# Performance work log

Hardware: AMD Instinct MI355X
Metric: run time of the kernel (lower is better)

## Reference

```python
import jax, jax.numpy as jnp
import numpy as np

NUM_CLS = 80
C = 256
IMG = 1024.0
N = 256
SR = 2  # sampling_ratio
MIN_SIZE = 16.0
SCALES = (0.25, 0.125, 0.0625, 0.03125)
HW = ((256, 256), (128, 128), (64, 64), (32, 32))


def _roialign(feat, rois, scale, out):
    # feat: [C, H, W]; rois: [n, 4] (y1, x1, y2, x2) in image coords.
    # torchvision-style ROIAlign (aligned=False), sampling_ratio=SR, avg pool.
    Cc, H, W = feat.shape
    n = rois.shape[0]
    y1 = rois[:, 0] * scale
    x1 = rois[:, 1] * scale
    rh = jnp.maximum(rois[:, 2] * scale - y1, 1.0)
    rw = jnp.maximum(rois[:, 3] * scale - x1, 1.0)
    # per-bin sample offsets: (bin + (s+0.5)/SR) * bin_size
    g = (jnp.arange(out, dtype=feat.dtype)[:, None]
         + (jnp.arange(SR, dtype=feat.dtype)[None, :] + 0.5) / SR).reshape(-1)  # [out*SR]
    ys = y1[:, None] + g[None, :] * (rh / out)[:, None]  # [n, out*SR]
    xs = x1[:, None] + g[None, :] * (rw / out)[:, None]
    S = out * SR
    yy = jnp.broadcast_to(ys[:, :, None], (n, S, S)).reshape(n, S * S)
    xx = jnp.broadcast_to(xs[:, None, :], (n, S, S)).reshape(n, S * S)
    valid = (yy > -1.0) & (yy < H) & (xx > -1.0) & (xx < W)
    yc = jnp.clip(yy, 0.0, H - 1.0)
    xc = jnp.clip(xx, 0.0, W - 1.0)
    y0 = jnp.floor(yc)
    x0 = jnp.floor(xc)
    ly = yc - y0
    lx = xc - x0
    y0i = y0.astype(jnp.int32)
    x0i = x0.astype(jnp.int32)
    y1i = jnp.minimum(y0i + 1, H - 1)
    x1i = jnp.minimum(x0i + 1, W - 1)
    f00 = feat[:, y0i, x0i]  # [C, n, S*S]
    f01 = feat[:, y0i, x1i]
    f10 = feat[:, y1i, x0i]
    f11 = feat[:, y1i, x1i]
    val = (f00 * (1 - ly) * (1 - lx) + f01 * (1 - ly) * lx
           + f10 * ly * (1 - lx) + f11 * ly * lx)
    val = jnp.where(valid[None], val, 0.0)
    val = val.reshape(Cc, n, out, SR, out, SR).mean(axis=(3, 5))
    return val.transpose(1, 0, 2, 3)  # [n, C, out, out]


def _pool(P, rois, out):
    # roi_layer: FPN level assignment via log2 of sqrt(area)/224, clamp to levels 0..3
    area = jnp.prod(rois[:, 2:4] - rois[:, 0:2] + 1.0, axis=-1)
    lvl = jnp.clip(jnp.floor(4.0 + jnp.log(jnp.sqrt(area) / 224.0) / np.log(2.0)), 2.0, 5.0) - 2.0
    lvl = lvl.astype(jnp.int32)
    pooled = jnp.zeros((rois.shape[0], C, out, out), dtype=rois.dtype)
    for l in range(4):
        pl = _roialign(P[l], rois, SCALES[l], out)
        pooled = pooled + jnp.where((lvl == l)[:, None, None, None], pl, 0.0)
    return pooled


def _loc2bbox(loc, anchor):
    chw = anchor[..., 2:4] - anchor[..., 0:2]
    cyx = anchor[..., 0:2] + chw * 0.5
    yx = loc[..., 0:2] * chw + cyx
    hw = jnp.exp(loc[..., 2:4]) * chw
    return jnp.concatenate([yx - hw * 0.5, yx + hw * 0.5], axis=-1)


def _head(x, W1, b1, W2, b2, Wc, bc, Wl, bl):
    x = x.reshape(x.shape[0], -1)
    h = jax.nn.relu(x @ W1 + b1)
    h = jax.nn.relu(h @ W2 + b2)
    return h @ Wc + bc, h @ Wl + bl


def _cascade(P, rois, params):
    stds = (jnp.array([0.1, 0.1, 0.2, 0.2], dtype=rois.dtype),
            jnp.array([0.05, 0.05, 0.1, 0.1], dtype=rois.dtype),
            jnp.array([1 / 30.0, 1 / 30.0, 1 / 15.0, 1 / 15.0], dtype=rois.dtype))
    roi = rois
    valid = jnp.ones((rois.shape[0],), dtype=bool)
    t = jnp.arange(rois.shape[0])
    pre_b = jnp.zeros((rois.shape[0], NUM_CLS, 4), dtype=rois.dtype)
    pre_s = jnp.zeros((rois.shape[0], NUM_CLS), dtype=rois.dtype)
    for s in range(3):
        x = _pool(P, roi, 7)
        logits, loc = _head(x, *params[s])
        loc = loc.reshape(-1, NUM_CLS + 1, 4)[:, 1:] * stds[s]
        boxes = _loc2bbox(loc, roi[:, None, :])  # [N, NUM_CLS, 4]
        score = jax.nn.softmax(logits, axis=-1)[:, 1:]
        pre_b = pre_b + boxes
        pre_s = pre_s + score
        best = jnp.argmax(score, axis=-1)
        roi = boxes[t, best]
        roi = jnp.clip(roi, 0.0, IMG)  # square image: clamp both coords to [0, IMG]
        if s < 2:  # original filters only after stages 1 and 2
            hw = roi[:, 2:4] - roi[:, 0:2]
            valid = valid & jnp.all(hw >= MIN_SIZE, axis=-1)
    m = valid.astype(pre_s.dtype)
    return pre_b / 3.0 * m[:, None, None], pre_s / 3.0 * m[:, None]


def setup_inputs():
    key = jax.random.key(0)
    ks = jax.random.split(key, 32)
    inp = {}
    for i, (h, w) in enumerate(HW):
        inp[f"P{i}"] = jax.random.normal(ks[i], (C, h, w), dtype=jnp.float32)
    yx1 = jax.random.uniform(ks[4], (N, 2), minval=0.0, maxval=IMG - 64.0)
    sz = jnp.exp(jax.random.uniform(ks[5], (N, 2), minval=np.log(16.0), maxval=np.log(600.0)))
    yx2 = jnp.clip(yx1 + sz, 0.0, IMG - 1.0)
    inp["rois"] = jnp.concatenate([yx1, yx2], axis=-1).astype(jnp.float32)
    dims = [(C * 49, 1024), (1024,), (1024, 1024), (1024,),
            (1024, NUM_CLS + 1), (NUM_CLS + 1,), (1024, (NUM_CLS + 1) * 4), ((NUM_CLS + 1) * 4,)]
    names = ["W1", "b1", "W2", "b2", "Wc", "bc", "Wl", "bl"]
    k = 6
    for s in range(3):
        for nm, d in zip(names, dims):
            if len(d) == 1:
                inp[f"s{s}_{nm}"] = jnp.zeros(d, dtype=jnp.float32)
            else:
                inp[f"s{s}_{nm}"] = 0.02 * jax.random.normal(ks[k], d, dtype=jnp.float32)
                k += 1
    return inp


def reference(P0, P1, P2, P3, rois,
              s0_W1, s0_b1, s0_W2, s0_b2, s0_Wc, s0_bc, s0_Wl, s0_bl,
              s1_W1, s1_b1, s1_W2, s1_b2, s1_Wc, s1_bc, s1_Wl, s1_bl,
              s2_W1, s2_b1, s2_W2, s2_b2, s2_Wc, s2_bc, s2_Wl, s2_bl):
    P = (P0, P1, P2, P3)
    params = [(s0_W1, s0_b1, s0_W2, s0_b2, s0_Wc, s0_bc, s0_Wl, s0_bl),
              (s1_W1, s1_b1, s1_W2, s1_b2, s1_Wc, s1_bc, s1_Wl, s1_bl),
              (s2_W1, s2_b1, s2_W2, s2_b2, s2_Wc, s2_bc, s2_Wl, s2_bl)]
    return _cascade(P, rois, params)
```

## Files before the change

kernel.cpp:

```cpp
#include <hip/hip_runtime.h>
#include <math.h>


#define NROI 256
#define NCLS 80
#define APITCH 40

typedef __attribute__((ext_vector_type(8))) short short8;
typedef __attribute__((ext_vector_type(4))) float f32x4;

__device__ __forceinline__ unsigned short f2bf(float f) {
  unsigned u = __builtin_bit_cast(unsigned, f);
  unsigned r = (u + 0x7FFFu + ((u >> 16) & 1u)) >> 16;
  return (unsigned short)r;
}
__device__ __forceinline__ float bf2f(unsigned short u) {
  return __builtin_bit_cast(float, (unsigned)u << 16);
}

__global__ __launch_bounds__(256) void prep_kernel(
    const float* __restrict__ P0, const float* __restrict__ P1,
    const float* __restrict__ P2, const float* __restrict__ P3,
    unsigned short* __restrict__ Pb0, unsigned short* __restrict__ Pb1,
    unsigned short* __restrict__ Pb2, unsigned short* __restrict__ Pb3,
    const float* __restrict__ W1a, const float* __restrict__ W1b,
    const float* __restrict__ W1c,
    const float* __restrict__ W2a, const float* __restrict__ W2b,
    const float* __restrict__ W2c,
    const float* __restrict__ Wca, const float* __restrict__ Wcb,
    const float* __restrict__ Wcc,
    const float* __restrict__ Wla, const float* __restrict__ Wlb,
    const float* __restrict__ Wlc,
    unsigned short* __restrict__ Wt1, unsigned short* __restrict__ Wt2,
    unsigned short* __restrict__ Wth) {
  __shared__ unsigned short tile[32][33];
  int bid = blockIdx.x;
  int t = threadIdx.x;
  int r = t >> 3;
  int c4 = (t & 7) * 4;

  float4 v;
  unsigned short* dptr;

  if (bid < 21760) {
    const float* S;
    unsigned short* D;
    int N, idx;
    if (bid < 16384)      { S = P0; D = Pb0; N = 65536; idx = bid; }
    else if (bid < 20480) { S = P1; D = Pb1; N = 16384; idx = bid - 16384; }
    else if (bid < 21504) { S = P2; D = Pb2; N = 4096;  idx = bid - 20480; }
    else                  { S = P3; D = Pb3; N = 1024;  idx = bid - 21504; }
    int k0 = (idx & 7) * 32;
    int n0 = (idx >> 3) * 32;
    v = *(const float4*)(S + (size_t)(k0 + r) * N + n0 + c4);
    dptr = D + (size_t)(n0 + r) * 256 + k0 + c4;
  } else if (bid < 59392) {
    int idx = bid - 21760;
    int s = idx / 12544;
    idx -= s * 12544;
    const float* W = (s == 0) ? W1a : (s == 1) ? W1b : W1c;
    int bx = idx % 392;
    int by = idx / 392;
    int kd0 = bx * 32;
    int n0 = by * 32;
    int p = kd0 >> 8;
    int c0 = kd0 & 255;
    v = *(const float4*)(W + (size_t)((c0 + r) * 49 + p) * 1024 + n0 + c4);
    dptr = Wt1 + (size_t)s * 12544 * 1024 + (size_t)(n0 + r) * 12544 + kd0 + c4;
  } else if (bid < 62464) {
    int idx = bid - 59392;
    int s = idx >> 10;
    idx &= 1023;
    const float* W = (s == 0) ? W2a : (s == 1) ? W2b : W2c;
    int k0 = (idx & 31) * 32;
    int n0 = (idx >> 5) * 32;
    v = *(const float4*)(W + (size_t)(k0 + r) * 1024 + n0 + c4);
    dptr = Wt2 + (size_t)s * 1024 * 1024 + (size_t)(n0 + r) * 1024 + k0 + c4;
  } else {
    int idx = bid - 62464;
    int s = idx >> 9;
    idx &= 511;
    const float* wc = (s == 0) ? Wca : (s == 1) ? Wcb : Wcc;
    const float* wl = (s == 0) ? Wla : (s == 1) ? Wlb : Wlc;
    int k0 = (idx & 31) * 32;
    int n0 = (idx >> 5) * 32;
    float vv[4];
#pragma unroll
    for (int j = 0; j < 4; j++) {
      int nn = n0 + c4 + j;
      float x = 0.0f;
      if (nn < 81) x = wc[(size_t)(k0 + r) * 81 + nn];
      else if (nn < 405) x = wl[(size_t)(k0 + r) * 324 + (nn - 81)];
      vv[j] = x;
    }
    v.x = vv[0]; v.y = vv[1]; v.z = vv[2]; v.w = vv[3];
    dptr = Wth + (size_t)s * 512 * 1024 + (size_t)(n0 + r) * 1024 + k0 + c4;
  }

  tile[r][c4 + 0] = f2bf(v.x);
  tile[r][c4 + 1] = f2bf(v.y);
  tile[r][c4 + 2] = f2bf(v.z);
  tile[r][c4 + 3] = f2bf(v.w);
  __syncthreads();
  struct __attribute__((aligned(8))) US4 { unsigned short a, b, c, d; } o;
  o.a = tile[c4 + 0][r];
  o.b = tile[c4 + 1][r];
  o.c = tile[c4 + 2][r];
  o.d = tile[c4 + 3][r];
  *(US4*)dptr = o;
}

__global__ __launch_bounds__(256) void pool_kernel2(
    const unsigned short* __restrict__ Pb0, const unsigned short* __restrict__ Pb1,
    const unsigned short* __restrict__ Pb2, const unsigned short* __restrict__ Pb3,
    const float* __restrict__ roi, unsigned short* __restrict__ pooled) {
  int t = threadIdx.x;
  int n = blockIdx.y;
  int p = blockIdx.x * 4 + (t >> 6);
  if (p >= 49) return;
  int lane = t & 63;
  int c4 = lane * 4;
  int py = p / 7, px = p % 7;

  float r0 = roi[n * 4 + 0];
  float r1 = roi[n * 4 + 1];
  float r2 = roi[n * 4 + 2];
  float r3 = roi[n * 4 + 3];

  float area = (r2 - r0 + 1.0f) * (r3 - r1 + 1.0f);
  float lf = floorf(4.0f + log2f(sqrtf(area) / 224.0f));
  lf = fminf(fmaxf(lf, 2.0f), 5.0f);
  int lvl = (int)lf - 2;

  float scale;
  int H;
  const unsigned short* fb;
  if (lvl == 0)      { scale = 0.25f;    H = 256; fb = Pb0; }
  else if (lvl == 1) { scale = 0.125f;   H = 128; fb = Pb1; }
  else if (lvl == 2) { scale = 0.0625f;  H = 64;  fb = Pb2; }
  else               { scale = 0.03125f; H = 32;  fb = Pb3; }
  int W = H;

  float y1 = r0 * scale;
  float x1 = r1 * scale;
  float rh = fmaxf(r2 * scale - y1, 1.0f);
  float rw = fmaxf(r3 * scale - x1, 1.0f);
  float bh = rh * (1.0f / 7.0f);
  float bw = rw * (1.0f / 7.0f);

  float a0 = 0.f, a1 = 0.f, a2 = 0.f, a3 = 0.f;
#pragma unroll
  for (int ry = 0; ry < 2; ry++) {
    float yy = y1 + ((float)py + ((float)ry + 0.5f) * 0.5f) * bh;
    bool vy = (yy > -1.0f) && (yy < (float)H);
    float ycl = fminf(fmaxf(yy, 0.0f), (float)(H - 1));
    float y0f = floorf(ycl);
    float ly = ycl - y0f;
    int y0i = (int)y0f;
    int y1i = min(y0i + 1, H - 1);
#pragma unroll
    for (int rx = 0; rx < 2; rx++) {
      float xx = x1 + ((float)px + ((float)rx + 0.5f) * 0.5f) * bw;
      bool vx = (xx > -1.0f) && (xx < (float)W);
      float xcl = fminf(fmaxf(xx, 0.0f), (float)(W - 1));
      float x0f = floorf(xcl);
      float lx = xcl - x0f;
      int x0i = (int)x0f;
      int x1i = min(x0i + 1, W - 1);
      float w00 = (1.f - ly) * (1.f - lx);
      float w01 = (1.f - ly) * lx;
      float w10 = ly * (1.f - lx);
      float w11 = ly * lx;
      if (!(vy && vx)) { w00 = w01 = w10 = w11 = 0.f; }
      ushort4 f00 = *(const ushort4*)(fb + ((size_t)(y0i * W + x0i) * 256 + c4));
      ushort4 f01 = *(const ushort4*)(fb + ((size_t)(y0i * W + x1i) * 256 + c4));
      ushort4 f10 = *(const ushort4*)(fb + ((size_t)(y1i * W + x0i) * 256 + c4));
      ushort4 f11 = *(const ushort4*)(fb + ((size_t)(y1i * W + x1i) * 256 + c4));
      a0 += bf2f(f00.x) * w00 + bf2f(f01.x) * w01 + bf2f(f10.x) * w10 + bf2f(f11.x) * w11;
      a1 += bf2f(f00.y) * w00 + bf2f(f01.y) * w01 + bf2f(f10.y) * w10 + bf2f(f11.y) * w11;
      a2 += bf2f(f00.z) * w00 + bf2f(f01.z) * w01 + bf2f(f10.z) * w10 + bf2f(f11.z) * w11;
      a3 += bf2f(f00.w) * w00 + bf2f(f01.w) * w01 + bf2f(f10.w) * w10 + bf2f(f11.w) * w11;
    }
  }
  ushort4 o;
  o.x = f2bf(a0 * 0.25f);
  o.y = f2bf(a1 * 0.25f);
  o.z = f2bf(a2 * 0.25f);
  o.w = f2bf(a3 * 0.25f);
  *(ushort4*)(pooled + (size_t)n * 12544 + p * 256 + c4) = o;
}

__global__ __launch_bounds__(256) void gemm_bf16(
    const unsigned short* __restrict__ A, const unsigned short* __restrict__ B,
    float* __restrict__ Cpart, int M, int N, int K, int iters) {
  __shared__ unsigned short As[128 * APITCH];
  __shared__ unsigned short Bs[128 * APITCH];
  const int t = threadIdx.x;
  const int n0 = blockIdx.x * 128;
  const int m0 = blockIdx.y * 128;
  const size_t kt0 = (size_t)blockIdx.z * iters * 32;

  const int row = t >> 2;
  const int off = (t & 3) * 8;
  const unsigned short* pa0 = A + (size_t)(m0 + row) * K + kt0 + off;
  const unsigned short* pa1 = pa0 + (size_t)64 * K;
  const unsigned short* pb0 = B + (size_t)(n0 + row) * K + kt0 + off;
  const unsigned short* pb1 = pb0 + (size_t)64 * K;

  const int lane = t & 63;
  const int wave = t >> 6;
  const int wm = (wave >> 1) * 64;
  const int wn = (wave & 1) * 64;
  const int fr = lane & 15;
  const int kq = (lane >> 4) * 8;

  f32x4 acc[4][4];
#pragma unroll
  for (int i = 0; i < 4; i++)
#pragma unroll
    for (int j = 0; j < 4; j++) acc[i][j] = (f32x4){0.f, 0.f, 0.f, 0.f};

  uint4 ra0 = *(const uint4*)pa0;
  uint4 ra1 = *(const uint4*)pa1;
  uint4 rb0 = *(const uint4*)pb0;
  uint4 rb1 = *(const uint4*)pb1;

  for (int it = 0; it < iters; ++it) {
    *(uint4*)&As[row * APITCH + off] = ra0;
    *(uint4*)&As[(row + 64) * APITCH + off] = ra1;
    *(uint4*)&Bs[row * APITCH + off] = rb0;
    *(uint4*)&Bs[(row + 64) * APITCH + off] = rb1;
    __syncthreads();
    if (it + 1 < iters) {
      int d = (it + 1) * 32;
      ra0 = *(const uint4*)(pa0 + d);
      ra1 = *(const uint4*)(pa1 + d);
      rb0 = *(const uint4*)(pb0 + d);
      rb1 = *(const uint4*)(pb1 + d);
    }
    short8 af[4], bfv[4];
#pragma unroll
    for (int f = 0; f < 4; f++)
      af[f] = *(const short8*)&As[(wm + f * 16 + fr) * APITCH + kq];
#pragma unroll
    for (int f = 0; f < 4; f++)
      bfv[f] = *(const short8*)&Bs[(wn + f * 16 + fr) * APITCH + kq];
#pragma unroll
    for (int fm = 0; fm < 4; fm++)
#pragma unroll
      for (int fn = 0; fn < 4; fn++)
        acc[fm][fn] = __builtin_amdgcn_mfma_f32_16x16x32_bf16(af[fm], bfv[fn],
                                                              acc[fm][fn], 0, 0, 0);
    __syncthreads();
  }

  float* Cp = Cpart + (size_t)blockIdx.z * M * N;
  const int colb = n0 + wn + fr;
  const int rowb = m0 + wm + (lane >> 4) * 4;
#pragma unroll
  for (int fm = 0; fm < 4; fm++)
#pragma unroll
    for (int fn = 0; fn < 4; fn++)
#pragma unroll
      for (int r = 0; r < 4; r++)
        Cp[(size_t)(rowb + fm * 16 + r) * N + (colb + fn * 16)] = acc[fm][fn][r];
}

__global__ __launch_bounds__(256) void reduce_bias_relu(
    const float* __restrict__ parts, int nparts, const float* __restrict__ bias,
    unsigned short* __restrict__ outb) {
  int i = blockIdx.x * 256 + threadIdx.x;
  float s = 0.0f;
  for (int p = 0; p < nparts; ++p) s += parts[(size_t)p * 262144 + i];
  s = fmaxf(s + bias[i & 1023], 0.0f);
  outb[i] = f2bf(s);
}

__global__ __launch_bounds__(128) void decode_kernel(
    const float* __restrict__ headp, const float* __restrict__ bc,
    const float* __restrict__ bl,
    const float* __restrict__ roi_in, float* __restrict__ roi_out,
    float* __restrict__ valid,
    float* __restrict__ pre_b, float* __restrict__ pre_s,
    float* __restrict__ out,
    float st0, float st1, float st2, float st3, int stage) {
  int n = blockIdx.x;
  int t = threadIdx.x;
  __shared__ float red[128];
  __shared__ int redi[128];
  __shared__ float sroi[4];
  __shared__ float boxes[NCLS][4];

  if (t < 4) sroi[t] = roi_in[n * 4 + t];
  float l = -INFINITY;
  if (t < 81) {
    float s = 0.f;
#pragma unroll
    for (int z = 0; z < 4; z++) s += headp[(size_t)z * 131072 + n * 512 + t];
    l = s + bc[t];
  }
  red[t] = l;
  __syncthreads();
#pragma unroll
  for (int s = 64; s > 0; s >>= 1) {
    if (t < s) red[t] = fmaxf(red[t], red[t + s]);
    __syncthreads();
  }
  float mx = red[0];
  __syncthreads();
  red[t] = (t < 81) ? expf(l - mx) : 0.0f;
  __syncthreads();
#pragma unroll
  for (int s = 64; s > 0; s >>= 1) {
    if (t < s) red[t] += red[t + s];
    __syncthreads();
  }
  float denom = red[0];
  __syncthreads();

  float score = -INFINITY;
  if (t < NCLS) {
    float lj = 0.f;
#pragma unroll
    for (int z = 0; z < 4; z++) lj += headp[(size_t)z * 131072 + n * 512 + (t + 1)];
    lj += bc[t + 1];
    score = expf(lj - mx) / denom;
    float lp[4];
#pragma unroll
    for (int j = 0; j < 4; j++) {
      float s = 0.f;
#pragma unroll
      for (int z = 0; z < 4; z++)
        s += headp[(size_t)z * 131072 + n * 512 + 81 + (t + 1) * 4 + j];
      lp[j] = s + bl[(t + 1) * 4 + j];
    }
    float dy = lp[0] * st0;
    float dx = lp[1] * st1;
    float dh = lp[2] * st2;
    float dw = lp[3] * st3;
    float h_ = sroi[2] - sroi[0];
    float w_ = sroi[3] - sroi[1];
    float cy = sroi[0] + h_ * 0.5f;
    float cx = sroi[1] + w_ * 0.5f;
    float ny = dy * h_ + cy;
    float nx = dx * w_ + cx;
    float nh = expf(dh) * h_;
    float nw = expf(dw) * w_;
    float b0 = ny - nh * 0.5f;
    float b1v = nx - nw * 0.5f;
    float b2v = ny + nh * 0.5f;
    float b3v = nx + nw * 0.5f;
    int o = (n * NCLS + t) * 4;
    if (stage == 0) {
      pre_b[o + 0] = b0;
      pre_b[o + 1] = b1v;
      pre_b[o + 2] = b2v;
      pre_b[o + 3] = b3v;
      pre_s[n * NCLS + t] = score;
    } else if (stage == 1) {
      pre_b[o + 0] += b0;
      pre_b[o + 1] += b1v;
      pre_b[o + 2] += b2v;
      pre_b[o + 3] += b3v;
      pre_s[n * NCLS + t] += score;
    } else {
      float vm = valid[n] * (1.0f / 3.0f);
      out[o + 0] = (pre_b[o + 0] + b0) * vm;
      out[o + 1] = (pre_b[o + 1] + b1v) * vm;
      out[o + 2] = (pre_b[o + 2] + b2v) * vm;
      out[o + 3] = (pre_b[o + 3] + b3v) * vm;
      out[NROI * NCLS * 4 + n * NCLS + t] = (pre_s[n * NCLS + t] + score) * vm;
    }
    if (stage < 2) {
      boxes[t][0] = b0;
      boxes[t][1] = b1v;
      boxes[t][2] = b2v;
      boxes[t][3] = b3v;
    }
  }
  if (stage < 2) {
    red[t] = score;
    redi[t] = t;
    __syncthreads();
    for (int s = 64; s > 0; s >>= 1) {
      if (t < s) {
        float o2 = red[t + s];
        int oi = redi[t + s];
        if (o2 > red[t] || (o2 == red[t] && oi < redi[t])) {
          red[t] = o2;
          redi[t] = oi;
        }
      }
      __syncthreads();
    }
    if (t == 0) {
      int best = redi[0];
      float ry1 = fminf(fmaxf(boxes[best][0], 0.0f), 1024.0f);
      float rx1 = fminf(fmaxf(boxes[best][1], 0.0f), 1024.0f);
      float ry2 = fminf(fmaxf(boxes[best][2], 0.0f), 1024.0f);
      float rx2 = fminf(fmaxf(boxes[best][3], 0.0f), 1024.0f);
      roi_out[n * 4 + 0] = ry1;
      roi_out[n * 4 + 1] = rx1;
      roi_out[n * 4 + 2] = ry2;
      roi_out[n * 4 + 3] = rx2;
      float hh = ry2 - ry1, ww = rx2 - rx1;
      bool ok = (hh >= 16.0f && ww >= 16.0f);
      if (stage == 0) valid[n] = ok ? 1.0f : 0.0f;
      else if (!ok) valid[n] = 0.0f;
    }
  }
}

extern "C" void kernel_launch(void* const* d_in, const int* in_sizes, int n_in,
                              void* d_out, int out_size, void* d_ws, size_t ws_size,
                              hipStream_t stream) {
  const float* P0 = (const float*)d_in[0];
  const float* P1 = (const float*)d_in[1];
  const float* P2 = (const float*)d_in[2];
  const float* P3 = (const float*)d_in[3];
  const float* rois = (const float*)d_in[4];
  float* out = (float*)d_out;
  float* ws = (float*)d_ws;

  float* roi   = ws;
  float* valid = roi + 1024;
  float* pre_b = valid + 256;
  float* pre_s = pre_b + 81920;
  float* part1 = pre_s + 20480;
  float* part2 = part1 + (size_t)14 * 262144;
  float* parth = part2 + (size_t)8 * 262144;
  unsigned short* pooledb = (unsigned short*)(parth + (size_t)4 * 131072);
  unsigned short* Wt1 = pooledb + (size_t)256 * 12544;
  unsigned short* Wt2 = Wt1 + (size_t)3 * 12544 * 1024;
  unsigned short* Wth = Wt2 + (size_t)3 * 1024 * 1024;
  unsigned short* h1b = Wth + (size_t)3 * 512 * 1024;
  unsigned short* h2b = h1b + (size_t)256 * 1024;
  unsigned short* Pb0 = h2b + (size_t)256 * 1024;
  unsigned short* Pb1 = Pb0 + (size_t)65536 * 256;
  unsigned short* Pb2 = Pb1 + (size_t)16384 * 256;
  unsigned short* Pb3 = Pb2 + (size_t)4096 * 256;

  prep_kernel<<<64000, 256, 0, stream>>>(
      P0, P1, P2, P3, Pb0, Pb1, Pb2, Pb3,
      (const float*)d_in[5 + 0 * 8 + 0], (const float*)d_in[5 + 1 * 8 + 0],
      (const float*)d_in[5 + 2 * 8 + 0],
      (const float*)d_in[5 + 0 * 8 + 2], (const float*)d_in[5 + 1 * 8 + 2],
      (const float*)d_in[5 + 2 * 8 + 2],
      (const float*)d_in[5 + 0 * 8 + 4], (const float*)d_in[5 + 1 * 8 + 4],
      (const float*)d_in[5 + 2 * 8 + 4],
      (const float*)d_in[5 + 0 * 8 + 6], (const float*)d_in[5 + 1 * 8 + 6],
      (const float*)d_in[5 + 2 * 8 + 6],
      Wt1, Wt2, Wth);

  const float stds[3][4] = {
      {0.1f, 0.1f, 0.2f, 0.2f},
      {0.05f, 0.05f, 0.1f, 0.1f},
      {1.0f / 30.0f, 1.0f / 30.0f, 1.0f / 15.0f, 1.0f / 15.0f}};

  for (int s = 0; s < 3; s++) {
    const float* b1 = (const float*)d_in[5 + s * 8 + 1];
    const float* b2 = (const float*)d_in[5 + s * 8 + 3];
    const float* bc = (const float*)d_in[5 + s * 8 + 5];
    const float* bl = (const float*)d_in[5 + s * 8 + 7];
    const float* roi_src = (s == 0) ? rois : roi;

    pool_kernel2<<<dim3(13, 256), 256, 0, stream>>>(Pb0, Pb1, Pb2, Pb3, roi_src,
                                                    pooledb);

    gemm_bf16<<<dim3(8, 2, 14), 256, 0, stream>>>(
        pooledb, Wt1 + (size_t)s * 12544 * 1024, part1, 256, 1024, 12544, 28);
    reduce_bias_relu<<<1024, 256, 0, stream>>>(part1, 14, b1, h1b);

    gemm_bf16<<<dim3(8, 2, 8), 256, 0, stream>>>(
        h1b, Wt2 + (size_t)s * 1024 * 1024, part2, 256, 1024, 1024, 4);
    reduce_bias_relu<<<1024, 256, 0, stream>>>(part2, 8, b2, h2b);

    gemm_bf16<<<dim3(4, 2, 4), 256, 0, stream>>>(
        h2b, Wth + (size_t)s * 512 * 1024, parth, 256, 512, 1024, 8);

    decode_kernel<<<256, 128, 0, stream>>>(parth, bc, bl, roi_src, roi, valid,
                                           pre_b, pre_s, out, stds[s][0],
                                           stds[s][1], stds[s][2], stds[s][3], s);
  }
}
```

Baseline: 481.3 us.

## Replace split-K GEMMs for FC2/head with fused bias-ReLU GEMM, widen prep tiles

Adds a 64x64-tile MFMA GEMM without split-K that applies bias and ReLU in its epilogue. It replaces the split-K FC2 GEMM plus reduce kernel and the split-K head GEMM, so decode now reads a single partial. This removes two launches per stage and the fp32 partial-buffer round trips, at the cost of fewer blocks in flight over the K=1024 loop. The prep transpose kernel also handles two 32x32 tiles per block with vectorized LDS writes, halving its block count.

Result: slower. 511.0 us (+6.2%).

```diff
diff --git a/kernel.cpp b/kernel.cpp
--- a/kernel.cpp
+++ b/kernel.cpp
@@ -17,6 +17,8 @@
 __device__ __forceinline__ float bf2f(unsigned short u) {
   return __builtin_bit_cast(float, (unsigned)u << 16);
 }
+
+struct __attribute__((aligned(8))) US4 { unsigned short a, b, c, d; };
 
 __global__ __launch_bounds__(256) void prep_kernel(
     const float* __restrict__ P0, const float* __restrict__ P1,
@@ -33,81 +35,103 @@
     const float* __restrict__ Wlc,
     unsigned short* __restrict__ Wt1, unsigned short* __restrict__ Wt2,
     unsigned short* __restrict__ Wth) {
-  __shared__ unsigned short tile[32][33];
+  __shared__ unsigned short tile[2][32][36];
   int bid = blockIdx.x;
   int t = threadIdx.x;
   int r = t >> 3;
   int c4 = (t & 7) * 4;
 
-  float4 v;
-  unsigned short* dptr;
-
-  if (bid < 21760) {
+  float4 v0, v1;
+  unsigned short *dp0, *dp1;
+
+  if (bid < 10880) {
     const float* S;
     unsigned short* D;
     int N, idx;
-    if (bid < 16384)      { S = P0; D = Pb0; N = 65536; idx = bid; }
-    else if (bid < 20480) { S = P1; D = Pb1; N = 16384; idx = bid - 16384; }
-    else if (bid < 21504) { S = P2; D = Pb2; N = 4096;  idx = bid - 20480; }
-    else                  { S = P3; D = Pb3; N = 1024;  idx = bid - 21504; }
+    if (bid < 8192)       { S = P0; D = Pb0; N = 65536; idx = bid; }
+    else if (bid < 10240) { S = P1; D = Pb1; N = 16384; idx = bid - 8192; }
+    else if (bid < 10752) { S = P2; D = Pb2; N = 4096;  idx = bid - 10240; }
+    else                  { S = P3; D = Pb3; N = 1024;  idx = bid - 10752; }
     int k0 = (idx & 7) * 32;
-    int n0 = (idx >> 3) * 32;
-    v = *(const float4*)(S + (size_t)(k0 + r) * N + n0 + c4);
-    dptr = D + (size_t)(n0 + r) * 256 + k0 + c4;
-  } else if (bid < 59392) {
-    int idx = bid - 21760;
-    int s = idx / 12544;
-    idx -= s * 12544;
+    int n0 = (idx >> 3) * 64;
+    const float* src = S + (size_t)(k0 + r) * N + n0 + c4;
+    v0 = *(const float4*)src;
+    v1 = *(const float4*)(src + 32);
+    dp0 = D + (size_t)(n0 + r) * 256 + k0 + c4;
+    dp1 = D + (size_t)(n0 + 32 + r) * 256 + k0 + c4;
+  } else if (bid < 29696) {
+    int idx = bid - 10880;
+    int s = idx / 6272;
+    idx -= s * 6272;
     const float* W = (s == 0) ? W1a : (s == 1) ? W1b : W1c;
     int bx = idx % 392;
-    int by = idx / 392;
+    int ny = idx / 392;
     int kd0 = bx * 32;
-    int n0 = by * 32;
+    int n0 = ny * 64;
     int p = kd0 >> 8;
     int c0 = kd0 & 255;
-    v = *(const float4*)(W + (size_t)((c0 + r) * 49 + p) * 1024 + n0 + c4);
-    dptr = Wt1 + (size_t)s * 12544 * 1024 + (size_t)(n0 + r) * 12544 + kd0 + c4;
-  } else if (bid < 62464) {
-    int idx = bid - 59392;
-    int s = idx >> 10;
-    idx &= 1023;
+    const float* src = W + (size_t)((c0 + r) * 49 + p) * 1024 + n0 + c4;
+    v0 = *(const float4*)src;
+    v1 = *(const float4*)(src + 32);
+    unsigned short* D = Wt1 + (size_t)s * 12544 * 1024;
+    dp0 = D + (size_t)(n0 + r) * 12544 + kd0 + c4;
+    dp1 = D + (size_t)(n0 + 32 + r) * 12544 + kd0 + c4;
+  } else if (bid < 31232) {
+    int idx = bid - 29696;
+    int s = idx >> 9;
+    idx &= 511;
     const float* W = (s == 0) ? W2a : (s == 1) ? W2b : W2c;
     int k0 = (idx & 31) * 32;
-    int n0 = (idx >> 5) * 32;
-    v = *(const float4*)(W + (size_t)(k0 + r) * 1024 + n0 + c4);
-    dptr = Wt2 + (size_t)s * 1024 * 1024 + (size_t)(n0 + r) * 1024 + k0 + c4;
+    int n0 = (idx >> 5) * 64;
+    const float* src = W + (size_t)(k0 + r) * 1024 + n0 + c4;
+    v0 = *(const float4*)src;
+    v1 = *(const float4*)(src + 32);
+    unsigned short* D = Wt2 + (size_t)s * 1024 * 1024;
+    dp0 = D + (size_t)(n0 + r) * 1024 + k0 + c4;
+    dp1 = D + (size_t)(n0 + 32 + r) * 1024 + k0 + c4;
   } else {
-    int idx = bid - 62464;
-    int s = idx >> 9;
-    idx &= 511;
+    int idx = bid - 31232;
+    int s = idx >> 8;
+    idx &= 255;
     const float* wc = (s == 0) ? Wca : (s == 1) ? Wcb : Wcc;
     const float* wl = (s == 0) ? Wla : (s == 1) ? Wlb : Wlc;
     int k0 = (idx & 31) * 32;
-    int n0 = (idx >> 5) * 32;
-    float vv[4];
-#pragma unroll
-    for (int j = 0; j < 4; j++) {
-      int nn = n0 + c4 + j;
-      float x = 0.0f;
-      if (nn < 81) x = wc[(size_t)(k0 + r) * 81 + nn];
-      else if (nn < 405) x = wl[(size_t)(k0 + r) * 324 + (nn - 81)];
-      vv[j] = x;
-    }
-    v.x = vv[0]; v.y = vv[1]; v.z = vv[2]; v.w = vv[3];
-    dptr = Wth + (size_t)s * 512 * 1024 + (size_t)(n0 + r) * 1024 + k0 + c4;
-  }
-
-  tile[r][c4 + 0] = f2bf(v.x);
-  tile[r][c4 + 1] = f2bf(v.y);
-  tile[r][c4 + 2] = f2bf(v.z);
-  tile[r][c4 + 3] = f2bf(v.w);
+    int n0 = (idx >> 5) * 64;
+    float a[2][4];
+#pragma unroll
+    for (int q = 0; q < 2; q++)
+#pragma unroll
+      for (int j = 0; j < 4; j++) {
+        int nn = n0 + q * 32 + c4 + j;
+        float x = 0.0f;
+        if (nn < 81) x = wc[(size_t)(k0 + r) * 81 + nn];
+        else if (nn < 405) x = wl[(size_t)(k0 + r) * 324 + (nn - 81)];
+        a[q][j] = x;
+      }
+    v0.x = a[0][0]; v0.y = a[0][1]; v0.z = a[0][2]; v0.w = a[0][3];
+    v1.x = a[1][0]; v1.y = a[1][1]; v1.z = a[1][2]; v1.w = a[1][3];
+    unsigned short* D = Wth + (size_t)s * 512 * 1024;
+    dp0 = D + (size_t)(n0 + r) * 1024 + k0 + c4;
+    dp1 = D + (size_t)(n0 + 32 + r) * 1024 + k0 + c4;
+  }
+
+  US4 w0, w1;
+  w0.a = f2bf(v0.x); w0.b = f2bf(v0.y); w0.c = f2bf(v0.z); w0.d = f2bf(v0.w);
+  w1.a = f2bf(v1.x); w1.b = f2bf(v1.y); w1.c = f2bf(v1.z); w1.d = f2bf(v1.w);
+  *(US4*)&tile[0][r][c4] = w0;
+  *(US4*)&tile[1][r][c4] = w1;
   __syncthreads();
-  struct __attribute__((aligned(8))) US4 { unsigned short a, b, c, d; } o;
-  o.a = tile[c4 + 0][r];
-  o.b = tile[c4 + 1][r];
-  o.c = tile[c4 + 2][r];
-  o.d = tile[c4 + 3][r];
-  *(US4*)dptr = o;
+  US4 o0, o1;
+  o0.a = tile[0][c4 + 0][r];
+  o0.b = tile[0][c4 + 1][r];
+  o0.c = tile[0][c4 + 2][r];
+  o0.d = tile[0][c4 + 3][r];
+  o1.a = tile[1][c4 + 0][r];
+  o1.b = tile[1][c4 + 1][r];
+  o1.c = tile[1][c4 + 2][r];
+  o1.d = tile[1][c4 + 3][r];
+  *(US4*)dp0 = o0;
+  *(US4*)dp1 = o1;
 }
 
 __global__ __launch_bounds__(256) void pool_kernel2(
@@ -266,6 +290,84 @@
         Cp[(size_t)(rowb + fm * 16 + r) * N + (colb + fn * 16)] = acc[fm][fn][r];
 }
 
+__global__ __launch_bounds__(256) void gemm_fused(
+    const unsigned short* __restrict__ A, const unsigned short* __restrict__ B,
+    const float* __restrict__ bias, float* __restrict__ outf,
+    unsigned short* __restrict__ outb, int N, int K, int mode) {
+  __shared__ unsigned short As[64 * APITCH];
+  __shared__ unsigned short Bs[64 * APITCH];
+  const int t = threadIdx.x;
+  const int n0 = blockIdx.x * 64;
+  const int m0 = blockIdx.y * 64;
+
+  const int row = t >> 2;
+  const int off = (t & 3) * 8;
+  const unsigned short* pa = A + (size_t)(m0 + row) * K + off;
+  const unsigned short* pb = B + (size_t)(n0 + row) * K + off;
+
+  const int lane = t & 63;
+  const int wave = t >> 6;
+  const int wm = (wave >> 1) * 32;
+  const int wn = (wave & 1) * 32;
+  const int fr = lane & 15;
+  const int kq = (lane >> 4) * 8;
+
+  f32x4 acc[2][2];
+#pragma unroll
+  for (int i = 0; i < 2; i++)
+#pragma unroll
+    for (int j = 0; j < 2; j++) acc[i][j] = (f32x4){0.f, 0.f, 0.f, 0.f};
+
+  uint4 ra = *(const uint4*)pa;
+  uint4 rb = *(const uint4*)pb;
+  const int iters = K / 32;
+
+  for (int it = 0; it < iters; ++it) {
+    *(uint4*)&As[row * APITCH + off] = ra;
+    *(uint4*)&Bs[row * APITCH + off] = rb;
+    __syncthreads();
+    if (it + 1 < iters) {
+      int d = (it + 1) * 32;
+      ra = *(const uint4*)(pa + d);
+      rb = *(const uint4*)(pb + d);
+    }
+    short8 af[2], bfv[2];
+#pragma unroll
+    for (int f = 0; f < 2; f++)
+      af[f] = *(const short8*)&As[(wm + f * 16 + fr) * APITCH + kq];
+#pragma unroll
+    for (int f = 0; f < 2; f++)
+      bfv[f] = *(const short8*)&Bs[(wn + f * 16 + fr) * APITCH + kq];
+#pragma unroll
+    for (int fm = 0; fm < 2; fm++)
+#pragma unroll
+      for (int fn = 0; fn < 2; fn++)
+        acc[fm][fn] = __builtin_amdgcn_mfma_f32_16x16x32_bf16(af[fm], bfv[fn],
+                                                              acc[fm][fn], 0, 0, 0);
+    __syncthreads();
+  }
+
+  const int colb = n0 + wn + fr;
+  const int rowb = m0 + wm + (lane >> 4) * 4;
+#pragma unroll
+  for (int fm = 0; fm < 2; fm++)
+#pragma unroll
+    for (int fn = 0; fn < 2; fn++) {
+      int col = colb + fn * 16;
+#pragma unroll
+      for (int r = 0; r < 4; r++) {
+        int rw = rowb + fm * 16 + r;
+        float s = acc[fm][fn][r];
+        if (mode == 0) {
+          s = fmaxf(s + bias[col], 0.0f);
+          outb[(size_t)rw * N + col] = f2bf(s);
+        } else {
+          outf[(size_t)rw * N + col] = s;
+        }
+      }
+    }
+}
+
 __global__ __launch_bounds__(256) void reduce_bias_relu(
     const float* __restrict__ parts, int nparts, const float* __restrict__ bias,
     unsigned short* __restrict__ outb) {
@@ -293,12 +395,7 @@
 
   if (t < 4) sroi[t] = roi_in[n * 4 + t];
   float l = -INFINITY;
-  if (t < 81) {
-    float s = 0.f;
-#pragma unroll
-    for (int z = 0; z < 4; z++) s += headp[(size_t)z * 131072 + n * 512 + t];
-    l = s + bc[t];
-  }
+  if (t < 81) l = headp[n * 512 + t] + bc[t];
   red[t] = l;
   __syncthreads();
 #pragma unroll
@@ -320,20 +417,12 @@
 
   float score = -INFINITY;
   if (t < NCLS) {
-    float lj = 0.f;
-#pragma unroll
-    for (int z = 0; z < 4; z++) lj += headp[(size_t)z * 131072 + n * 512 + (t + 1)];
-    lj += bc[t + 1];
+    float lj = headp[n * 512 + (t + 1)] + bc[t + 1];
     score = expf(lj - mx) / denom;
     float lp[4];
 #pragma unroll
-    for (int j = 0; j < 4; j++) {
-      float s = 0.f;
-#pragma unroll
-      for (int z = 0; z < 4; z++)
-        s += headp[(size_t)z * 131072 + n * 512 + 81 + (t + 1) * 4 + j];
-      lp[j] = s + bl[(t + 1) * 4 + j];
-    }
+    for (int j = 0; j < 4; j++)
+      lp[j] = headp[n * 512 + 81 + (t + 1) * 4 + j] + bl[(t + 1) * 4 + j];
     float dy = lp[0] * st0;
     float dx = lp[1] * st1;
     float dh = lp[2] * st2;
@@ -427,9 +516,8 @@
   float* pre_b = valid + 256;
   float* pre_s = pre_b + 81920;
   float* part1 = pre_s + 20480;
-  float* part2 = part1 + (size_t)14 * 262144;
-  float* parth = part2 + (size_t)8 * 262144;
-  unsigned short* pooledb = (unsigned short*)(parth + (size_t)4 * 131072);
+  float* parth = part1 + (size_t)14 * 262144;
+  unsigned short* pooledb = (unsigned short*)(parth + 131072);
   unsigned short* Wt1 = pooledb + (size_t)256 * 12544;
   unsigned short* Wt2 = Wt1 + (size_t)3 * 12544 * 1024;
   unsigned short* Wth = Wt2 + (size_t)3 * 1024 * 1024;
@@ -440,7 +528,7 @@
   unsigned short* Pb2 = Pb1 + (size_t)16384 * 256;
   unsigned short* Pb3 = Pb2 + (size_t)4096 * 256;
 
-  prep_kernel<<<64000, 256, 0, stream>>>(
+  prep_kernel<<<32000, 256, 0, stream>>>(
       P0, P1, P2, P3, Pb0, Pb1, Pb2, Pb3,
       (const float*)d_in[5 + 0 * 8 + 0], (const float*)d_in[5 + 1 * 8 + 0],
       (const float*)d_in[5 + 2 * 8 + 0],
@@ -471,12 +559,11 @@
         pooledb, Wt1 + (size_t)s * 12544 * 1024, part1, 256, 1024, 12544, 28);
     reduce_bias_relu<<<1024, 256, 0, stream>>>(part1, 14, b1, h1b);
 
-    gemm_bf16<<<dim3(8, 2, 8), 256, 0, stream>>>(
-        h1b, Wt2 + (size_t)s * 1024 * 1024, part2, 256, 1024, 1024, 4);
-    reduce_bias_relu<<<1024, 256, 0, stream>>>(part2, 8, b2, h2b);
-
-    gemm_bf16<<<dim3(4, 2, 4), 256, 0, stream>>>(
-        h2b, Wth + (size_t)s * 512 * 1024, parth, 256, 512, 1024, 8);
+    gemm_fused<<<dim3(16, 4), 256, 0, stream>>>(
+        h1b, Wt2 + (size_t)s * 1024 * 1024, b2, nullptr, h2b, 1024, 1024, 0);
+
+    gemm_fused<<<dim3(8, 4), 256, 0, stream>>>(
+        h2b, Wth + (size_t)s * 512 * 1024, nullptr, parth, nullptr, 512, 1024, 1);
 
     decode_kernel<<<256, 128, 0, stream>>>(parth, bc, bl, roi_src, roi, valid,
                                            pre_b, pre_s, out, stds[s][0],
```
